# Performance work log

Measured on AMD Instinct MI355X. Metric: run time of the kernel, lower is better.

## Reference

```python
import jax, jax.numpy as jnp
import numpy as np

T, B, H, L = 512, 128, 256, 2  # seq_len, batch, hidden(=input) size, num_layers


def setup_inputs() -> dict:
    key = jax.random.key(0)
    k0, k1, k2, k3, k4 = jax.random.split(key, 5)
    s = 1.0 / np.sqrt(H)  # PyTorch LSTM init range
    x = jax.random.normal(k0, (T, B, H), jnp.float32)
    W_ih = jax.random.uniform(k1, (L, 4 * H, H), jnp.float32, -s, s)
    W_hh = jax.random.uniform(k2, (L, 4 * H, H), jnp.float32, -s, s)
    b_ih = jax.random.uniform(k3, (L, 4 * H), jnp.float32, -s, s)
    b_hh = jax.random.uniform(k4, (L, 4 * H), jnp.float32, -s, s)
    return {"x": x, "W_ih": W_ih, "W_hh": W_hh, "b_ih": b_ih, "b_hh": b_hh}


def _lstm(x, W_ih, W_hh, b_ih, b_hh):
    Ln, fourH, _ = W_ih.shape
    Hh = fourH // 4
    Bn = x.shape[1]
    h0 = jnp.zeros((Ln, Bn, Hh), x.dtype)
    c0 = jnp.zeros((Ln, Bn, Hh), x.dtype)

    def step(carry, x_t):
        h, c = carry
        inp = x_t
        hs, cs = [], []
        for l in range(Ln):  # small static layer loop
            gates = inp @ W_ih[l].T + b_ih[l] + h[l] @ W_hh[l].T + b_hh[l]
            gi, gf, gg, go = jnp.split(gates, 4, axis=-1)
            gi = jax.nn.sigmoid(gi)
            gf = jax.nn.sigmoid(gf)
            gg = jnp.tanh(gg)
            go = jax.nn.sigmoid(go)
            c_new = gf * c[l] + gi * gg
            h_new = go * jnp.tanh(c_new)
            hs.append(h_new)
            cs.append(c_new)
            inp = h_new
        return (jnp.stack(hs), jnp.stack(cs)), inp

    (hT, cT), out = jax.lax.scan(step, (h0, c0), x)
    return out, hT, cT


def reference(x, W_ih, W_hh, b_ih, b_hh):
    # Returns (output [T,B,H], h_n [L,B,H], c_n [L,B,H]) as in DPLSTM.forward
    return _lstm(x, W_ih, W_hh, b_ih, b_hh)
```

## Files before the change

kernel.cpp:

```cpp
#include <hip/hip_runtime.h>
#include <math.h>

#define T_LEN 512
#define BATCH 128
#define HID   256
#define BH    (BATCH*HID)

__device__ __forceinline__ float sigmoid_f(float v) {
    return 1.f / (1.f + __expf(-v));
}
__device__ __forceinline__ float tanh_f(float v) {
    v = fminf(fmaxf(v, -15.f), 15.f);
    float e = __expf(2.f * v);
    return (e - 1.f) / (e + 1.f);
}
__device__ __forceinline__ float4 ldf4(const float* p) {
    return *reinterpret_cast<const float4*>(p);
}
__device__ __forceinline__ void fma4(float4& a, const float4 v, const float4 w) {
    a.x = fmaf(v.x, w.x, a.x);
    a.y = fmaf(v.y, w.y, a.y);
    a.z = fmaf(v.z, w.z, a.z);
    a.w = fmaf(v.w, w.w, a.w);
}
__device__ __forceinline__ float hsum4(const float4 a) {
    return (a.x + a.y) + (a.z + a.w);
}
__device__ __forceinline__ void pin4(float4& v) {
    asm volatile("" : "+v"(v.x), "+v"(v.y), "+v"(v.z), "+v"(v.w));
}
__device__ __forceinline__ void astore(float* p, float v) {
    __hip_atomic_store(p, v, __ATOMIC_RELAXED, __HIP_MEMORY_SCOPE_AGENT);
}
__device__ __forceinline__ float2 af2(const float* p) {
    unsigned long long u = __hip_atomic_load((const unsigned long long*)p,
                                             __ATOMIC_RELAXED, __HIP_MEMORY_SCOPE_AGENT);
    union { unsigned long long u; float2 f; } c; c.u = u;
    return c.f;
}
__device__ __forceinline__ float4 af4(const float* p) {
    const float2 a = af2(p), b = af2(p + 2);
    return make_float4(a.x, a.y, b.x, b.y);
}
template<int CTRL>
__device__ __forceinline__ float dpp_mv(float x) {
    return __int_as_float(__builtin_amdgcn_update_dpp(
        0, __float_as_int(x), CTRL, 0xF, 0xF, true));
}
__device__ __forceinline__ float red16(float x) {
    x += dpp_mv<0x111>(x);
    x += dpp_mv<0x112>(x);
    x += dpp_mv<0x114>(x);
    x += dpp_mv<0x118>(x);
    return x;
}

__global__ __launch_bounds__(256)
__attribute__((amdgpu_waves_per_eu(2, 2)))
void lstm_persist(
    const float* __restrict__ x,
    const float* __restrict__ Wih, const float* __restrict__ Whh,
    const float* __restrict__ bih, const float* __restrict__ bhh,
    float* __restrict__ out,
    float* __restrict__ h0buf,
    float* __restrict__ h1buf,
    int* __restrict__ flags)
{
    __shared__ float ls_in[8 * 576];
    __shared__ float ls_c[128];
    __shared__ float ls_a[128 * 4];

    const int tid = threadIdx.x;
    const int bid = blockIdx.x;
    const int bg = bid & 15;
    const int layer = (bid >> 4) & 1;
    const int jt = bid >> 5;
    const int jp = tid >> 4;
    const int kc = tid & 15;
    const int j = jt * 16 + jp;
    const int Bg0 = bg * 8;

    const float* Wih_l = Wih + (size_t)layer * 4 * HID * HID;
    const float* Whh_l = Whh + (size_t)layer * 4 * HID * HID;
    const float* bih_l = bih + layer * 4 * HID;
    const float* bhh_l = bhh + layer * 4 * HID;

    float4 w[4][8];
    float bias[4];
    #pragma unroll
    for (int g = 0; g < 4; ++g) {
        const int row = g * HID + j;
        const float* base = (kc < 8)
            ? (Wih_l + (size_t)row * HID + kc * 32)
            : (Whh_l + (size_t)row * HID + (kc - 8) * 32);
        #pragma unroll
        for (int m = 0; m < 8; ++m) {
            w[g][m] = ldf4(base + m * 4);
            pin4(w[g][m]);
        }
        bias[g] = bih_l[row] + bhh_l[row];
        asm volatile("" : "+v"(bias[g]));
    }

    if (tid < 128) ls_c[tid] = 0.f;

    int* myflag = flags + bg * 32 + layer * 16 + jt;

    #pragma unroll 1
    for (int s = 0; s <= T_LEN; ++s) {
        if (s > 0 && tid < 32) {
            const int* f = flags + bg * 32 + tid;
            while (__hip_atomic_load(f, __ATOMIC_RELAXED, __HIP_MEMORY_SCOPE_AGENT) < s)
                __builtin_amdgcn_s_sleep(1);
        }
        __syncthreads();

        const bool active = (layer == 0) ? (s < T_LEN) : (s >= 1);
        if (active) {
            const bool zero2 = (layer == 0) ? (s == 0) : (s == 1);
            const float* p1 = (layer == 0)
                ? (x + (size_t)s * BH)
                : (h0buf + (size_t)((s + 2) % 3) * BH);
            const float* p2 = (layer == 0)
                ? (h0buf + (size_t)((s + 2) % 3) * BH)
                : (h1buf + (size_t)((s + 1) % 3) * BH);
            #pragma unroll
            for (int i = 0; i < 4; ++i) {
                const int F = tid + 256 * i;
                const int b = F >> 7;
                const int rr = F & 127;
                const int col = (rr & 63) * 4;
                float4 v;
                if ((rr >> 6) == 0) {
                    const float* src = p1 + (size_t)(Bg0 + b) * HID + col;
                    v = (layer == 0) ? ldf4(src) : af4(src);
                } else if (zero2) {
                    v = make_float4(0.f, 0.f, 0.f, 0.f);
                } else {
                    const float* src = p2 + (size_t)(Bg0 + b) * HID + col;
                    v = af4(src);
                }
                *(float4*)(ls_in + b * 576 + (rr >> 3) * 36 + (rr & 7) * 4) = v;
            }
        }
        __syncthreads();

        if (active) {
            #pragma unroll 1
            for (int b = 0; b < 8; ++b) {
                const float* Lp = ls_in + b * 576 + kc * 36;
                float4 in[8];
                #pragma unroll
                for (int m = 0; m < 8; ++m) in[m] = *(const float4*)(Lp + m * 4);
                float4 ac[4];
                #pragma unroll
                for (int g = 0; g < 4; ++g) ac[g] = make_float4(0.f, 0.f, 0.f, 0.f);
                #pragma unroll
                for (int m = 0; m < 8; ++m) {
                    #pragma unroll
                    for (int g = 0; g < 4; ++g) fma4(ac[g], in[m], w[g][m]);
                }
                float a0 = red16(hsum4(ac[0]));
                float a1 = red16(hsum4(ac[1]));
                float a2 = red16(hsum4(ac[2]));
                float a3 = red16(hsum4(ac[3]));
                if (kc == 15) {
                    float* ap = ls_a + (b * 16 + jp) * 4;
                    ap[0] = a0 + bias[0];
                    ap[1] = a1 + bias[1];
                    ap[2] = a2 + bias[2];
                    ap[3] = a3 + bias[3];
                }
            }
        }
        __syncthreads();

        if (active && tid < 128) {
            const int bb = tid >> 4;
            const int jpp = tid & 15;
            const int t_s = (layer == 0) ? s : (s - 1);
            float* hst = ((layer == 0) ? h0buf : h1buf) + (size_t)(t_s % 3) * BH;
            const bool last = (layer == 0) ? (s == T_LEN - 1) : (s == T_LEN);
            const float* ap = ls_a + tid * 4;
            const float gi = sigmoid_f(ap[0]);
            const float gf = sigmoid_f(ap[1]);
            const float gg = tanh_f   (ap[2]);
            const float go = sigmoid_f(ap[3]);
            const float cold = ls_c[tid];
            const float cnew = fmaf(gf, cold, gi * gg);
            ls_c[tid] = cnew;
            const float h = go * tanh_f(cnew);
            const int B = Bg0 + bb;
            const int jg = jt * 16 + jpp;
            astore(hst + (size_t)B * HID + jg, h);
            if (layer == 1)
                out[(size_t)t_s * BH + (size_t)B * HID + jg] = h;
            if (last) {
                float* hn  = out + (size_t)T_LEN * BH;
                float* cnp = hn + 2 * BH;
                hn [(size_t)layer * BH + (size_t)B * HID + jg] = h;
                cnp[(size_t)layer * BH + (size_t)B * HID + jg] = cnew;
            }
        }
        __syncthreads();
        if (s < T_LEN && tid == 0)
            __hip_atomic_store(myflag, s + 1, __ATOMIC_RELAXED, __HIP_MEMORY_SCOPE_AGENT);
    }
}

extern "C" void kernel_launch(void* const* d_in, const int* in_sizes, int n_in,
                              void* d_out, int out_size, void* d_ws, size_t ws_size,
                              hipStream_t stream) {
    const float* x   = (const float*)d_in[0];
    const float* Wih = (const float*)d_in[1];
    const float* Whh = (const float*)d_in[2];
    const float* bih = (const float*)d_in[3];
    const float* bhh = (const float*)d_in[4];
    float* out = (float*)d_out;

    float* h0 = (float*)d_ws;
    float* h1 = h0 + 3 * BH;
    int* flags = (int*)(h1 + 3 * BH);

    hipLaunchKernelGGL(lstm_persist, dim3(512), dim3(256), 0, stream,
                       x, Wih, Whh, bih, bhh, out, h0, h1, flags);
}
```

Measured before the change: 3.735 ms.

## Split input and recurrent matvecs, computing input projection off the critical path

Splits each block's weights into separate input and hidden halves. The input projection (W_ih·x) for the next step is computed after the flag is published and stashed in shared memory. The recurrent step then only does the W_hh·h part before the gate update. The pipeline is re-timed: layer 1 lags by three steps and the layer-0 wait on layer-1 flags is relaxed. The aim is to shorten the serial dependency chain per step, at the cost of extra loop iterations and more complex flag and buffer indexing.

```diff
diff --git a/kernel.cpp b/kernel.cpp
--- a/kernel.cpp
+++ b/kernel.cpp
@@ -67,8 +67,9 @@
     int* __restrict__ flags)
 {
     __shared__ float ls_in[8 * 576];
-    __shared__ float ls_c[128];
-    __shared__ float ls_a[128 * 4];
+    __shared__ float ls_a [128 * 4];
+    __shared__ float ls_ax[128 * 4];
+    __shared__ float ls_c [128];
 
     const int tid = threadIdx.x;
     const int bid = blockIdx.x;
@@ -85,18 +86,19 @@
     const float* bih_l = bih + layer * 4 * HID;
     const float* bhh_l = bhh + layer * 4 * HID;
 
-    float4 w[4][8];
+    float4 wih[4][4], whh[4][4];
     float bias[4];
     #pragma unroll
     for (int g = 0; g < 4; ++g) {
         const int row = g * HID + j;
-        const float* base = (kc < 8)
-            ? (Wih_l + (size_t)row * HID + kc * 32)
-            : (Whh_l + (size_t)row * HID + (kc - 8) * 32);
+        const float* pih = Wih_l + (size_t)row * HID + kc * 16;
+        const float* phh = Whh_l + (size_t)row * HID + kc * 16;
         #pragma unroll
-        for (int m = 0; m < 8; ++m) {
-            w[g][m] = ldf4(base + m * 4);
-            pin4(w[g][m]);
+        for (int m = 0; m < 4; ++m) {
+            wih[g][m] = ldf4(pih + m * 4);
+            pin4(wih[g][m]);
+            whh[g][m] = ldf4(phh + m * 4);
+            pin4(whh[g][m]);
         }
         bias[g] = bih_l[row] + bhh_l[row];
         asm volatile("" : "+v"(bias[g]));
@@ -107,80 +109,82 @@
     int* myflag = flags + bg * 32 + layer * 16 + jt;
 
     #pragma unroll 1
-    for (int s = 0; s <= T_LEN; ++s) {
+    for (int s = 0; s <= T_LEN + 2; ++s) {
         if (s > 0 && tid < 32) {
+            const int thr = (layer == 0 && tid >= 16) ? (s - 1) : s;
             const int* f = flags + bg * 32 + tid;
-            while (__hip_atomic_load(f, __ATOMIC_RELAXED, __HIP_MEMORY_SCOPE_AGENT) < s)
+            while (__hip_atomic_load(f, __ATOMIC_RELAXED, __HIP_MEMORY_SCOPE_AGENT) < thr)
                 __builtin_amdgcn_s_sleep(1);
         }
         __syncthreads();
 
-        const bool active = (layer == 0) ? (s < T_LEN) : (s >= 1);
-        if (active) {
-            const bool zero2 = (layer == 0) ? (s == 0) : (s == 1);
-            const float* p1 = (layer == 0)
-                ? (x + (size_t)s * BH)
-                : (h0buf + (size_t)((s + 2) % 3) * BH);
-            const float* p2 = (layer == 0)
-                ? (h0buf + (size_t)((s + 2) % 3) * BH)
-                : (h1buf + (size_t)((s + 1) % 3) * BH);
+        const bool crit = (layer == 0) ? (s >= 1 && s <= T_LEN) : (s >= 3);
+        const bool xact = (layer == 0) ? (s < T_LEN) : (s >= 2 && s <= T_LEN + 1);
+        const bool zeroh = (layer == 0) ? (s == 1) : (s == 3);
+
+        if (crit || xact) {
+            const float* ph0 = h0buf + (size_t)((s + 1) % 3) * BH;
+            const float* ph1 = h1buf + (size_t)((s + 2) % 3) * BH;
             #pragma unroll
             for (int i = 0; i < 4; ++i) {
                 const int F = tid + 256 * i;
                 const int b = F >> 7;
                 const int rr = F & 127;
                 const int col = (rr & 63) * 4;
-                float4 v;
+                const size_t row = (size_t)(Bg0 + b) * HID + col;
+                float4 v = make_float4(0.f, 0.f, 0.f, 0.f);
                 if ((rr >> 6) == 0) {
-                    const float* src = p1 + (size_t)(Bg0 + b) * HID + col;
-                    v = (layer == 0) ? ldf4(src) : af4(src);
-                } else if (zero2) {
-                    v = make_float4(0.f, 0.f, 0.f, 0.f);
-                } else {
-                    const float* src = p2 + (size_t)(Bg0 + b) * HID + col;
-                    v = af4(src);
+                    if (xact)
+                        v = (layer == 0) ? ldf4(x + (size_t)s * BH + row)
+                                         : af4(ph0 + row);
+                } else if (crit && !zeroh) {
+                    v = (layer == 0) ? af4(ph0 + row) : af4(ph1 + row);
                 }
                 *(float4*)(ls_in + b * 576 + (rr >> 3) * 36 + (rr & 7) * 4) = v;
             }
         }
         __syncthreads();
 
-        if (active) {
-            #pragma unroll 1
+        if (crit) {
+            #pragma unroll 2
             for (int b = 0; b < 8; ++b) {
-                const float* Lp = ls_in + b * 576 + kc * 36;
-                float4 in[8];
-                #pragma unroll
-                for (int m = 0; m < 8; ++m) in[m] = *(const float4*)(Lp + m * 4);
+                const float4* Lp = (const float4*)(ls_in + b * 576 + 288
+                                                   + (kc >> 1) * 36 + (kc & 1) * 16);
+                float4 in[4];
+                #pragma unroll
+                for (int m = 0; m < 4; ++m) in[m] = Lp[m];
                 float4 ac[4];
                 #pragma unroll
                 for (int g = 0; g < 4; ++g) ac[g] = make_float4(0.f, 0.f, 0.f, 0.f);
                 #pragma unroll
-                for (int m = 0; m < 8; ++m) {
+                for (int m = 0; m < 4; ++m) {
                     #pragma unroll
-                    for (int g = 0; g < 4; ++g) fma4(ac[g], in[m], w[g][m]);
-                }
-                float a0 = red16(hsum4(ac[0]));
-                float a1 = red16(hsum4(ac[1]));
-                float a2 = red16(hsum4(ac[2]));
-                float a3 = red16(hsum4(ac[3]));
+                    for (int g = 0; g < 4; ++g) fma4(ac[g], in[m], whh[g][m]);
+                }
+                const float a0 = red16(hsum4(ac[0]));
+                const float a1 = red16(hsum4(ac[1]));
+                const float a2 = red16(hsum4(ac[2]));
+                const float a3 = red16(hsum4(ac[3]));
                 if (kc == 15) {
-                    float* ap = ls_a + (b * 16 + jp) * 4;
-                    ap[0] = a0 + bias[0];
-                    ap[1] = a1 + bias[1];
-                    ap[2] = a2 + bias[2];
-                    ap[3] = a3 + bias[3];
-                }
-            }
-        }
-        __syncthreads();
-
-        if (active && tid < 128) {
+                    const int cell = b * 16 + jp;
+                    const float* axp = ls_ax + cell * 4;
+                    float* ap = ls_a + cell * 4;
+                    ap[0] = a0 + bias[0] + axp[0];
+                    ap[1] = a1 + bias[1] + axp[1];
+                    ap[2] = a2 + bias[2] + axp[2];
+                    ap[3] = a3 + bias[3] + axp[3];
+                }
+            }
+        }
+        __syncthreads();
+
+        if (crit && tid < 128) {
             const int bb = tid >> 4;
             const int jpp = tid & 15;
-            const int t_s = (layer == 0) ? s : (s - 1);
-            float* hst = ((layer == 0) ? h0buf : h1buf) + (size_t)(t_s % 3) * BH;
-            const bool last = (layer == 0) ? (s == T_LEN - 1) : (s == T_LEN);
+            const int t = (layer == 0) ? (s - 1) : (s - 3);
+            float* hst = (layer == 0) ? (h0buf + (size_t)((s + 2) % 3) * BH)
+                                      : (h1buf + (size_t)(s % 3) * BH);
+            const bool last = (t == T_LEN - 1);
             const float* ap = ls_a + tid * 4;
             const float gi = sigmoid_f(ap[0]);
             const float gf = sigmoid_f(ap[1]);
@@ -194,7 +198,7 @@
             const int jg = jt * 16 + jpp;
             astore(hst + (size_t)B * HID + jg, h);
             if (layer == 1)
-                out[(size_t)t_s * BH + (size_t)B * HID + jg] = h;
+                out[(size_t)t * BH + (size_t)B * HID + jg] = h;
             if (last) {
                 float* hn  = out + (size_t)T_LEN * BH;
                 float* cnp = hn + 2 * BH;
@@ -203,8 +207,38 @@
             }
         }
         __syncthreads();
-        if (s < T_LEN && tid == 0)
+        if (s <= T_LEN + 1 && tid == 0)
             __hip_atomic_store(myflag, s + 1, __ATOMIC_RELAXED, __HIP_MEMORY_SCOPE_AGENT);
+
+        if (xact) {
+            #pragma unroll 2
+            for (int b = 0; b < 8; ++b) {
+                const float4* Lp = (const float4*)(ls_in + b * 576
+                                                   + (kc >> 1) * 36 + (kc & 1) * 16);
+                float4 in[4];
+                #pragma unroll
+                for (int m = 0; m < 4; ++m) in[m] = Lp[m];
+                float4 ac[4];
+                #pragma unroll
+                for (int g = 0; g < 4; ++g) ac[g] = make_float4(0.f, 0.f, 0.f, 0.f);
+                #pragma unroll
+                for (int m = 0; m < 4; ++m) {
+                    #pragma unroll
+                    for (int g = 0; g < 4; ++g) fma4(ac[g], in[m], wih[g][m]);
+                }
+                const float a0 = red16(hsum4(ac[0]));
+                const float a1 = red16(hsum4(ac[1]));
+                const float a2 = red16(hsum4(ac[2]));
+                const float a3 = red16(hsum4(ac[3]));
+                if (kc == 15) {
+                    float* axp = ls_ax + (b * 16 + jp) * 4;
+                    axp[0] = a0;
+                    axp[1] = a1;
+                    axp[2] = a2;
+                    axp[3] = a3;
+                }
+            }
+        }
     }
 }
 
```

Result: faster. 3.624 ms (-3.0%).
